# Optimization experiments

Hardware: AMD Instinct MI355X
Metric: run time of the kernel (lower is better)

The kernel has to match this reference:

```python
import jax, jax.numpy as jnp
import numpy as np

B, N, IN_DIM = 64, 4096, 128
D = 128          # slot_size
S = 7            # num_slots
ITERS = 3
HID = 256        # mlp_hdim
EPS = 1e-8       # renorm epsilon
LN_EPS = 1e-5    # torch LayerNorm default


def _ln(x, g, b):
    m = jnp.mean(x, axis=-1, keepdims=True)
    v = jnp.mean((x - m) ** 2, axis=-1, keepdims=True)
    return (x - m) * jax.lax.rsqrt(v + LN_EPS) * g + b


def setup_inputs() -> dict:
    key = jax.random.key(0)
    ks = jax.random.split(key, 16)
    s = 0.02
    return {
        "x": jax.random.normal(ks[0], (B, N, IN_DIM), jnp.float32),
        "noise": jax.random.normal(ks[1], (B, S, D), jnp.float32),
        "Wq": jax.random.normal(ks[2], (D, D), jnp.float32) * s,
        "Wk": jax.random.normal(ks[3], (D, IN_DIM), jnp.float32) * s,
        "Wv": jax.random.normal(ks[4], (D, IN_DIM), jnp.float32) * s,
        "ln_in_g": jnp.ones((IN_DIM,), jnp.float32),
        "ln_in_b": jnp.zeros((IN_DIM,), jnp.float32),
        "ln_slots_g": jnp.ones((D,), jnp.float32),
        "ln_slots_b": jnp.zeros((D,), jnp.float32),
        "ln_mlp_g": jnp.ones((D,), jnp.float32),
        "ln_mlp_b": jnp.zeros((D,), jnp.float32),
        "W_ih": jax.random.normal(ks[5], (3 * D, D), jnp.float32) * s,
        "W_hh": jax.random.normal(ks[6], (3 * D, D), jnp.float32) * s,
        "b_ih": jnp.zeros((3 * D,), jnp.float32),
        "b_hh": jnp.zeros((3 * D,), jnp.float32),
        "W1": jax.random.normal(ks[7], (HID, D), jnp.float32) * s,
        "b1": jnp.zeros((HID,), jnp.float32),
        "W2": jax.random.normal(ks[8], (D, HID), jnp.float32) * s,
        "b2": jnp.zeros((D,), jnp.float32),
        "mu": jax.random.normal(ks[9], (1, 1, D), jnp.float32) * s,
        "logsigma": jax.random.normal(ks[10], (1, D), jnp.float32) * s,
    }


def reference(x, noise, Wq, Wk, Wv, ln_in_g, ln_in_b, ln_slots_g, ln_slots_b,
              ln_mlp_g, ln_mlp_b, W_ih, W_hh, b_ih, b_hh, W1, b1, W2, b2,
              mu, logsigma):
    xn = _ln(x, ln_in_g, ln_in_b)              # (B,N,IN)
    k = xn @ Wk.T                              # (B,N,D)
    v = xn @ Wv.T                              # (B,N,D)

    scale = jax.nn.softplus(logsigma)[None] + 1e-5   # (1,1,D)
    slots = mu + scale * noise                 # rsample, (B,S,D)

    def gru(u, h):
        gx = u @ W_ih.T + b_ih                 # (B*S, 3D)
        gh = h @ W_hh.T + b_hh
        xr, xz, xn_ = jnp.split(gx, 3, axis=-1)
        hr, hz, hn = jnp.split(gh, 3, axis=-1)
        r = jax.nn.sigmoid(xr + hr)
        z = jax.nn.sigmoid(xz + hz)
        n = jnp.tanh(xn_ + r * hn)
        return (1.0 - z) * n + z * h

    inv_sqrt_d = D ** -0.5
    for _ in range(ITERS):
        slots_prev = slots
        sn = _ln(slots, ln_slots_g, ln_slots_b)
        q = sn @ Wq.T                          # (B,S,D)
        scores = inv_sqrt_d * jnp.einsum('bnd,bsd->bns', k, q)
        attn = jax.nn.softmax(scores, axis=-1)           # over slots
        attn = attn + EPS
        attn = attn / jnp.sum(attn, axis=1, keepdims=True)  # renorm over inputs
        updates = jnp.einsum('bns,bnd->bsd', attn, v)    # (B,S,D)
        h = gru(updates.reshape(-1, D), slots_prev.reshape(-1, D))
        slots = h.reshape(x.shape[0], S, D)
        slots = _ln(slots, ln_mlp_g, ln_mlp_b)
        slots = slots + (jax.nn.relu(slots @ W1.T + b1) @ W2.T + b2)
    return slots
```

## Files before the change

### kernel.cpp

```cpp
#include <hip/hip_runtime.h>
#include <hip/hip_bf16.h>
#include <stdint.h>

#define B_ 64
#define N_ 4096
#define D_ 128
#define S_ 7
#define EPS_ 1e-8f
#define LN_EPS_ 1e-5f
#define SC_INV 0.08838834764831843f

typedef float  f32x4  __attribute__((ext_vector_type(4)));
typedef __bf16 bf16x8 __attribute__((ext_vector_type(8)));

#define WIH_OFF 0
#define WHH_OFF 49152
#define W1_OFF  98304
#define W2_OFF  131072
#define WQ_OFF  163840
#define WKT_OFF 180224
#define WV_OFF  196608
#define WBF_TOT 212992

__device__ __forceinline__ uint16_t f2bfbits(float f) {
    uint32_t x = __float_as_uint(f);
    return (uint16_t)((x + 0x7fffu + ((x >> 16) & 1u)) >> 16);
}
__device__ __forceinline__ uint32_t pk2(float a, float b) {
    return (uint32_t)f2bfbits(a) | ((uint32_t)f2bfbits(b) << 16);
}

__global__ __launch_bounds__(256) void k_init_prep(
    const float* __restrict__ noise, const float* __restrict__ Wk,
    const float* __restrict__ mu, const float* __restrict__ logsigma,
    const float* __restrict__ Wq, const float* __restrict__ lsg,
    const float* __restrict__ lsb,
    const float* __restrict__ Wih, const float* __restrict__ Whh,
    const float* __restrict__ W1, const float* __restrict__ W2,
    const float* __restrict__ Wv,
    float* __restrict__ slots, uint16_t* __restrict__ kqbf,
    uint16_t* __restrict__ wbf,
    const float* __restrict__ x, const float* __restrict__ lng,
    const float* __restrict__ lnb, uint16_t* __restrict__ xn) {
    const int t = threadIdx.x;
    if (blockIdx.x < 448) {
        __shared__ float sn[128], qr[128];
        __shared__ float red[2];
        const int tid = blockIdx.x * 256 + t;
        const int row = blockIdx.x;
        const int b = row / 7, s = row - b * 7;
        bool act = t < 128;
        float v = 0.f;
        if (act) {
            float sc = log1pf(__expf(logsigma[t])) + 1e-5f;
            v = mu[t] + sc * noise[row * 128 + t];
            slots[row * 128 + t] = v;
        }
        float sv = act ? v : 0.f;
        #pragma unroll
        for (int m = 1; m < 64; m <<= 1) sv += __shfl_xor(sv, m);
        if (act && (t & 63) == 0) red[t >> 6] = sv;
        __syncthreads();
        float mean = (red[0] + red[1]) * (1.0f / 128.0f);
        __syncthreads();
        float dv = act ? (v - mean) : 0.f;
        float sq = dv * dv;
        #pragma unroll
        for (int m = 1; m < 64; m <<= 1) sq += __shfl_xor(sq, m);
        if (act && (t & 63) == 0) red[t >> 6] = sq;
        __syncthreads();
        float var = (red[0] + red[1]) * (1.0f / 128.0f);
        if (act) sn[t] = dv * rsqrtf(var + LN_EPS_) * lsg[t] + lsb[t];
        __syncthreads();
        if (act) {
            const float4* wr = (const float4*)(Wq + t * 128);
            float acc = 0.f;
            #pragma unroll 8
            for (int j = 0; j < 32; ++j) {
                float4 w = wr[j];
                float4 s4 = *(const float4*)(sn + 4 * j);
                acc += w.x * s4.x + w.y * s4.y + w.z * s4.z + w.w * s4.w;
            }
            qr[t] = acc;
        }
        __syncthreads();
        if (act) {
            float kq = 0.f;
            #pragma unroll 8
            for (int o = 0; o < 128; ++o) kq += qr[o] * Wk[o * 128 + t];
            int elem = (t >> 5) * 512 + (s + 16 * ((t >> 3) & 3)) * 8 + (t & 7);
            kqbf[b * 2048 + elem] = f2bfbits(kq * SC_INV);
        }
        if (tid < 73728) {
            int bb = tid / 1152, rem = tid - bb * 1152;
            int sp = 7 + (rem >> 7), d = rem & 127;
            int elem = (d >> 5) * 512 + (sp + 16 * ((d >> 3) & 3)) * 8 + (d & 7);
            kqbf[bb * 2048 + elem] = 0;
        }
        for (int e = tid; e < WBF_TOT; e += 448 * 256) {
            const float* W; int C, el, mode = 0;
            if (e < WHH_OFF)      { W = Wih; C = 128; el = e; }
            else if (e < W1_OFF)  { W = Whh; C = 128; el = e - WHH_OFF; }
            else if (e < W2_OFF)  { W = W1;  C = 128; el = e - W1_OFF; }
            else if (e < WQ_OFF)  { W = W2;  C = 256; el = e - W2_OFF; }
            else if (e < WKT_OFF) { W = Wq;  C = 128; el = e - WQ_OFF; }
            else if (e < WV_OFF)  { W = Wk;  C = 128; el = e - WKT_OFF; mode = 1; }
            else                  { W = Wv;  C = 128; el = e - WV_OFF; }
            int tile = el >> 9, within = el & 511;
            int lp = within >> 3, j = within & 7;
            int lm_ = lp & 15, qd_ = lp >> 4;
            float w;
            if (!mode) {
                int ktN = C >> 5, ot = tile / ktN, kt = tile - ot * ktN;
                w = W[(ot * 16 + lm_) * C + kt * 32 + qd_ * 8 + j];
            } else {
                int dt = tile >> 2, kt = tile & 3;
                w = W[(kt * 32 + qd_ * 8 + j) * 128 + dt * 16 + lm_];
            }
            wbf[e] = f2bfbits(w);
        }
        return;
    }
    const int pid = blockIdx.x - 448;
    const int wv = t >> 6, lane = t & 63;
    const int lm = lane & 15, qd = lane >> 4;
    const long row = (long)pid * 64 + wv * 16 + lm;
    const long ntile = (long)pid * 4 + wv;
    const float* xp = x + row * 128 + qd * 4;
    f32x4 xa[8];
    #pragma unroll
    for (int c = 0; c < 8; ++c) xa[c] = *(const f32x4*)(xp + c * 16);
    float s = 0.f, sq = 0.f;
    #pragma unroll
    for (int c = 0; c < 8; ++c)
        #pragma unroll
        for (int r = 0; r < 4; ++r) { float v = xa[c][r]; s += v; sq += v * v; }
    s  += __shfl_xor(s, 16);  s  += __shfl_xor(s, 32);
    sq += __shfl_xor(sq, 16); sq += __shfl_xor(sq, 32);
    float mean = s * (1.0f / 128.0f);
    float var  = sq * (1.0f / 128.0f) - mean * mean;
    float rs   = rsqrtf(var + LN_EPS_);
    #pragma unroll
    for (int c = 0; c < 8; ++c) {
        f32x4 g  = *(const f32x4*)(lng + c * 16 + qd * 4);
        f32x4 bb = *(const f32x4*)(lnb + c * 16 + qd * 4);
        float v0 = (xa[c][0] - mean) * rs * g[0] + bb[0];
        float v1 = (xa[c][1] - mean) * rs * g[1] + bb[1];
        float v2 = (xa[c][2] - mean) * rs * g[2] + bb[2];
        float v3 = (xa[c][3] - mean) * rs * g[3] + bb[3];
        uint2 st; st.x = pk2(v0, v1); st.y = pk2(v2, v3);
        long elem = (ntile * 4 + (c >> 1)) * 512
                  + (lm + 16 * (2 * (c & 1) + (qd >> 1))) * 8 + 4 * (qd & 1);
        *(uint2*)(xn + elem) = st;
    }
}

__global__ __launch_bounds__(256, 4) void k_attn(
    const uint16_t* __restrict__ xn, const uint16_t* __restrict__ kqbf,
    float* __restrict__ upart, float* __restrict__ cpart) {
    __shared__ __align__(16) uint16_t stage[4][32 * 132];
    __shared__ __align__(16) uint16_t als[4][16 * 36];
    __shared__ float bsum[4][8];
    const int t = threadIdx.x, wv = t >> 6, lane = t & 63;
    const int lm = lane & 15, qd = lane >> 4;
    const int b = blockIdx.x >> 4, chunk = blockIdx.x & 15;
    const int ntb = b * 256 + chunk * 16 + wv * 4;
    const int sbase = qd * 4;

    bf16x8 kqf[4];
    #pragma unroll
    for (int k0 = 0; k0 < 4; ++k0)
        kqf[k0] = *(const bf16x8*)(kqbf + b * 2048 + k0 * 512 + lane * 8);

    uint16_t* xw = stage[wv];
    float* prt = (float*)stage[wv];
    uint16_t* aw = als[wv];
    f32x4 uacc[8];
    #pragma unroll
    for (int i = 0; i < 8; ++i) uacc[i] = (f32x4){0.f, 0.f, 0.f, 0.f};
    f32x4 csl = {0.f, 0.f, 0.f, 0.f};

    #pragma unroll
    for (int sub = 0; sub < 2; ++sub) {
        bf16x8 xf[2][4];
        #pragma unroll
        for (int nt = 0; nt < 2; ++nt)
            #pragma unroll
            for (int k0 = 0; k0 < 4; ++k0)
                xf[nt][k0] = *(const bf16x8*)(xn +
                    ((long)(ntb + sub * 2 + nt) * 4 + k0) * 512 + lane * 8);
        #pragma unroll
        for (int nt = 0; nt < 2; ++nt)
            #pragma unroll
            for (int k0 = 0; k0 < 4; ++k0) {
                int base = (nt * 16 + lm) * 132 + k0 * 32 + qd * 8;
                const uint2* src = (const uint2*)&xf[nt][k0];
                *(uint2*)(xw + base)     = src[0];
                *(uint2*)(xw + base + 4) = src[1];
            }
        f32x4 sc[2];
        #pragma unroll
        for (int nt = 0; nt < 2; ++nt) {
            f32x4 acc = {0.f, 0.f, 0.f, 0.f};
            #pragma unroll
            for (int k0 = 0; k0 < 4; ++k0)
                acc = __builtin_amdgcn_mfma_f32_16x16x32_bf16(kqf[k0], xf[nt][k0], acc, 0, 0, 0);
            sc[nt] = acc;
        }
        #pragma unroll
        for (int nt = 0; nt < 2; ++nt) {
            float mx = -1e30f;
            #pragma unroll
            for (int r = 0; r < 4; ++r)
                if (sbase + r < 7) mx = fmaxf(mx, sc[nt][r]);
            mx = fmaxf(mx, __shfl_xor(mx, 16));
            mx = fmaxf(mx, __shfl_xor(mx, 32));
            float e[4], tot = 0.f;
            #pragma unroll
            for (int r = 0; r < 4; ++r) {
                e[r] = (sbase + r < 7) ? __expf(sc[nt][r] - mx) : 0.f;
                tot += e[r];
            }
            tot += __shfl_xor(tot, 16);
            tot += __shfl_xor(tot, 32);
            float inv = 1.0f / tot;
            #pragma unroll
            for (int r = 0; r < 4; ++r) {
                float a_ = (sbase + r < 7) ? e[r] * inv + EPS_ : 0.f;
                csl[r] += a_;
                aw[(sbase + r) * 36 + nt * 16 + lm] = f2bfbits(a_);
            }
        }
        union { uint2 u[2]; bf16x8 v; } cva;
        cva.u[0] = *(const uint2*)(aw + lm * 36 + qd * 8);
        cva.u[1] = *(const uint2*)(aw + lm * 36 + qd * 8 + 4);
        bf16x8 afr = cva.v;
        #pragma unroll
        for (int dt = 0; dt < 8; ++dt) {
            bf16x8 bfr;
            #pragma unroll
            for (int j = 0; j < 8; ++j)
                bfr[j] = ((const __bf16*)xw)[(qd * 8 + j) * 132 + dt * 16 + lm];
            uacc[dt] = __builtin_amdgcn_mfma_f32_16x16x32_bf16(afr, bfr, uacc[dt], 0, 0, 0);
        }
    }
    #pragma unroll
    for (int m = 1; m < 16; m <<= 1) {
        csl[0] += __shfl_xor(csl[0], m);
        csl[1] += __shfl_xor(csl[1], m);
        csl[2] += __shfl_xor(csl[2], m);
        csl[3] += __shfl_xor(csl[3], m);
    }
    if (lm == 0) {
        #pragma unroll
        for (int r = 0; r < 4; ++r) {
            int s = sbase + r;
            if (s < 7) bsum[wv][s] = csl[r];
        }
    }
    #pragma unroll
    for (int dt = 0; dt < 8; ++dt)
        #pragma unroll
        for (int r = 0; r < 4; ++r) {
            int s = sbase + r;
            if (s < 7) prt[s * 132 + dt * 16 + lm] = uacc[dt][r];
        }
    __syncthreads();
    if (t < 128) {
        const float* p0 = (const float*)stage[0];
        const float* p1 = (const float*)stage[1];
        const float* p2 = (const float*)stage[2];
        const float* p3 = (const float*)stage[3];
        #pragma unroll
        for (int s = 0; s < 7; ++s) {
            int o = s * 132 + t;
            upart[((b * 16 + chunk) * 7 + s) * 128 + t] = p0[o] + p1[o] + p2[o] + p3[o];
        }
    }
    if (t < 7)
        cpart[(b * 16 + chunk) * 7 + t] = bsum[0][t] + bsum[1][t] + bsum[2][t] + bsum[3][t];
}

__global__ __launch_bounds__(256) void k_fused(
    const float* __restrict__ upart, const float* __restrict__ cpart,
    float* __restrict__ slots, const uint16_t* __restrict__ wbf,
    const float* __restrict__ bih, const float* __restrict__ bhh,
    const float* __restrict__ gm, const float* __restrict__ bm,
    const float* __restrict__ b1, const float* __restrict__ b2,
    const float* __restrict__ lsg, const float* __restrict__ lsb,
    uint16_t* __restrict__ kqbf, float* __restrict__ dst, int hasq) {
    __shared__ float uf[16][132];
    __shared__ float hf[16][132];
    __shared__ float slf[16][132];
    __shared__ float hidl[16][264];
    __shared__ float glg[7][776];
    __shared__ float csl[7];
    const int b = blockIdx.x;
    const int t = threadIdx.x, wv = t >> 6, lane = t & 63;
    const int lm = lane & 15, qd = lane >> 4;

    if (t < 7) {
        float c = 0.f;
        #pragma unroll
        for (int i = 0; i < 16; ++i) c += cpart[(b * 16 + i) * 7 + t];
        csl[t] = c;
    }
    for (int idx = t; idx < 896; idx += 256) {
        int s = idx >> 7, d = idx & 127;
        float acc = 0.f;
        #pragma unroll
        for (int i = 0; i < 16; ++i) acc += upart[((b * 16 + i) * 7 + s) * 128 + d];
        slf[s][d] = acc;
        hf[s][d] = slots[(b * 7 + s) * 128 + d];
    }
    __syncthreads();

    {
        bf16x8 apb[4];
        #pragma unroll
        for (int k0 = 0; k0 < 4; ++k0)
            #pragma unroll
            for (int j = 0; j < 8; ++j) apb[k0][j] = (__bf16)slf[lm][k0 * 32 + qd * 8 + j];
        #pragma unroll
        for (int i = 0; i < 2; ++i) {
            int dt = wv * 2 + i;
            f32x4 acc = {0.f, 0.f, 0.f, 0.f};
            #pragma unroll
            for (int k0 = 0; k0 < 4; ++k0) {
                bf16x8 bf = *(const bf16x8*)(wbf + WV_OFF + ((dt * 4 + k0) << 9) + lane * 8);
                acc = __builtin_amdgcn_mfma_f32_16x16x32_bf16(apb[k0], bf, acc, 0, 0, 0);
            }
            #pragma unroll
            for (int r = 0; r < 4; ++r) {
                int s = qd * 4 + r;
                if (s < 7) uf[s][dt * 16 + lm] = acc[r] / csl[s];
            }
        }
    }
    __syncthreads();

    bf16x8 au[4], ah[4];
    #pragma unroll
    for (int k0 = 0; k0 < 4; ++k0)
        #pragma unroll
        for (int j = 0; j < 8; ++j) {
            au[k0][j] = (__bf16)uf[lm][k0 * 32 + qd * 8 + j];
            ah[k0][j] = (__bf16)hf[lm][k0 * 32 + qd * 8 + j];
        }
    {
        const int ih = (wv < 2);
        const uint16_t* W = wbf + (ih ? WIH_OFF : WHH_OFF);
        const int base = ih ? 0 : 384;
        const int w2 = wv & 1;
        #pragma unroll
        for (int i = 0; i < 12; ++i) {
            int ot = w2 * 12 + i;
            f32x4 acc = {0.f, 0.f, 0.f, 0.f};
            #pragma unroll
            for (int k0 = 0; k0 < 4; ++k0) {
                bf16x8 bf = *(const bf16x8*)(W + ((ot * 4 + k0) << 9) + lane * 8);
                acc = __builtin_amdgcn_mfma_f32_16x16x32_bf16(ih ? au[k0] : ah[k0], bf, acc, 0, 0, 0);
            }
            #pragma unroll
            for (int r = 0; r < 4; ++r) {
                int s = qd * 4 + r;
                if (s < 7) glg[s][base + ot * 16 + lm] = acc[r];
            }
        }
    }
    __syncthreads();

    for (int idx = t; idx < 896; idx += 256) {
        int s = idx >> 7, d = idx & 127;
        float xr = glg[s][d] + bih[d];
        float xz = glg[s][128 + d] + bih[128 + d];
        float xg = glg[s][256 + d] + bih[256 + d];
        float hr = glg[s][384 + d] + bhh[d];
        float hz = glg[s][512 + d] + bhh[128 + d];
        float hg = glg[s][640 + d] + bhh[256 + d];
        float r = 1.f / (1.f + __expf(-(xr + hr)));
        float z = 1.f / (1.f + __expf(-(xz + hz)));
        float n = tanhf(xg + r * hg);
        uf[s][d] = (1.f - z) * n + z * hf[s][d];
    }
    __syncthreads();

    for (int s = wv; s < 7; s += 4) {
        float a0 = uf[s][2 * lane], a1 = uf[s][2 * lane + 1];
        float sm = a0 + a1, sq = a0 * a0 + a1 * a1;
        #pragma unroll
        for (int m = 1; m < 64; m <<= 1) { sm += __shfl_xor(sm, m); sq += __shfl_xor(sq, m); }
        float mean = sm * (1.0f / 128.0f);
        float var = sq * (1.0f / 128.0f) - mean * mean;
        float rs = rsqrtf(var + LN_EPS_);
        slf[s][2 * lane]     = (a0 - mean) * rs * gm[2 * lane] + bm[2 * lane];
        slf[s][2 * lane + 1] = (a1 - mean) * rs * gm[2 * lane + 1] + bm[2 * lane + 1];
    }
    __syncthreads();

    bf16x8 as_[4];
    #pragma unroll
    for (int k0 = 0; k0 < 4; ++k0)
        #pragma unroll
        for (int j = 0; j < 8; ++j) as_[k0][j] = (__bf16)slf[lm][k0 * 32 + qd * 8 + j];
    #pragma unroll
    for (int i = 0; i < 4; ++i) {
        int ot = wv * 4 + i;
        f32x4 acc = {0.f, 0.f, 0.f, 0.f};
        #pragma unroll
        for (int k0 = 0; k0 < 4; ++k0) {
            bf16x8 bf = *(const bf16x8*)(wbf + W1_OFF + ((ot * 4 + k0) << 9) + lane * 8);
            acc = __builtin_amdgcn_mfma_f32_16x16x32_bf16(as_[k0], bf, acc, 0, 0, 0);
        }
        #pragma unroll
        for (int r = 0; r < 4; ++r) {
            int s = qd * 4 + r;
            if (s < 7) hidl[s][ot * 16 + lm] = fmaxf(acc[r] + b1[ot * 16 + lm], 0.f);
        }
    }
    __syncthreads();

    bf16x8 ahd[8];
    #pragma unroll
    for (int k0 = 0; k0 < 8; ++k0)
        #pragma unroll
        for (int j = 0; j < 8; ++j) ahd[k0][j] = (__bf16)hidl[lm][k0 * 32 + qd * 8 + j];
    #pragma unroll
    for (int i = 0; i < 2; ++i) {
        int ot = wv * 2 + i;
        f32x4 acc = {0.f, 0.f, 0.f, 0.f};
        #pragma unroll
        for (int k0 = 0; k0 < 8; ++k0) {
            bf16x8 bf = *(const bf16x8*)(wbf + W2_OFF + ((ot * 8 + k0) << 9) + lane * 8);
            acc = __builtin_amdgcn_mfma_f32_16x16x32_bf16(ahd[k0], bf, acc, 0, 0, 0);
        }
        #pragma unroll
        for (int r = 0; r < 4; ++r) {
            int s = qd * 4 + r;
            if (s < 7) {
                float v = slf[s][ot * 16 + lm] + acc[r] + b2[ot * 16 + lm];
                hf[s][ot * 16 + lm] = v;
                dst[(b * 7 + s) * 128 + ot * 16 + lm] = v;
            }
        }
    }
    if (hasq) {
        __syncthreads();
        for (int s = wv; s < 7; s += 4) {
            float a0 = hf[s][2 * lane], a1 = hf[s][2 * lane + 1];
            float sm = a0 + a1, sq = a0 * a0 + a1 * a1;
            #pragma unroll
            for (int m = 1; m < 64; m <<= 1) { sm += __shfl_xor(sm, m); sq += __shfl_xor(sq, m); }
            float mean = sm * (1.0f / 128.0f);
            float var = sq * (1.0f / 128.0f) - mean * mean;
            float rs = rsqrtf(var + LN_EPS_);
            uf[s][2 * lane]     = (a0 - mean) * rs * lsg[2 * lane] + lsb[2 * lane];
            uf[s][2 * lane + 1] = (a1 - mean) * rs * lsg[2 * lane + 1] + lsb[2 * lane + 1];
        }
        __syncthreads();
        bf16x8 an[4];
        #pragma unroll
        for (int k0 = 0; k0 < 4; ++k0)
            #pragma unroll
            for (int j = 0; j < 8; ++j) an[k0][j] = (__bf16)uf[lm][k0 * 32 + qd * 8 + j];
        #pragma unroll
        for (int i = 0; i < 2; ++i) {
            int ot = wv * 2 + i;
            f32x4 acc = {0.f, 0.f, 0.f, 0.f};
            #pragma unroll
            for (int k0 = 0; k0 < 4; ++k0) {
                bf16x8 bf = *(const bf16x8*)(wbf + WQ_OFF + ((ot * 4 + k0) << 9) + lane * 8);
                acc = __builtin_amdgcn_mfma_f32_16x16x32_bf16(an[k0], bf, acc, 0, 0, 0);
            }
            #pragma unroll
            for (int r = 0; r < 4; ++r) {
                int s = qd * 4 + r;
                if (s < 7) slf[s][ot * 16 + lm] = acc[r];
            }
        }
        __syncthreads();
        bf16x8 aq[4];
        #pragma unroll
        for (int k0 = 0; k0 < 4; ++k0)
            #pragma unroll
            for (int j = 0; j < 8; ++j) aq[k0][j] = (__bf16)slf[lm][k0 * 32 + qd * 8 + j];
        #pragma unroll
        for (int i = 0; i < 2; ++i) {
            int dt = wv * 2 + i;
            f32x4 acc = {0.f, 0.f, 0.f, 0.f};
            #pragma unroll
            for (int k0 = 0; k0 < 4; ++k0) {
                bf16x8 bf = *(const bf16x8*)(wbf + WKT_OFF + ((dt * 4 + k0) << 9) + lane * 8);
                acc = __builtin_amdgcn_mfma_f32_16x16x32_bf16(aq[k0], bf, acc, 0, 0, 0);
            }
            #pragma unroll
            for (int r = 0; r < 4; ++r) {
                int s = qd * 4 + r;
                if (s < 7) hidl[s][dt * 16 + lm] = acc[r];
            }
        }
        __syncthreads();
        {
            int kt = t >> 6, lp = t & 63;
            int lmp = lp & 15, qdp = lp >> 4;
            uint16_t h[8];
            #pragma unroll
            for (int j = 0; j < 8; ++j)
                h[j] = (lmp < 7) ? f2bfbits(hidl[lmp][kt * 32 + qdp * 8 + j] * SC_INV) : (uint16_t)0;
            uint4 st;
            st.x = (uint32_t)h[0] | ((uint32_t)h[1] << 16);
            st.y = (uint32_t)h[2] | ((uint32_t)h[3] << 16);
            st.z = (uint32_t)h[4] | ((uint32_t)h[5] << 16);
            st.w = (uint32_t)h[6] | ((uint32_t)h[7] << 16);
            *(uint4*)(kqbf + b * 2048 + t * 8) = st;
        }
    }
}

extern "C" void kernel_launch(void* const* d_in, const int* in_sizes, int n_in,
                              void* d_out, int out_size, void* d_ws, size_t ws_size,
                              hipStream_t stream) {
    const float* x    = (const float*)d_in[0];
    const float* nz   = (const float*)d_in[1];
    const float* Wq   = (const float*)d_in[2];
    const float* Wk   = (const float*)d_in[3];
    const float* Wv   = (const float*)d_in[4];
    const float* ling = (const float*)d_in[5];
    const float* linb = (const float*)d_in[6];
    const float* lsg  = (const float*)d_in[7];
    const float* lsb  = (const float*)d_in[8];
    const float* lmg  = (const float*)d_in[9];
    const float* lmb  = (const float*)d_in[10];
    const float* Wih  = (const float*)d_in[11];
    const float* Whh  = (const float*)d_in[12];
    const float* bih  = (const float*)d_in[13];
    const float* bhh  = (const float*)d_in[14];
    const float* W1   = (const float*)d_in[15];
    const float* b1   = (const float*)d_in[16];
    const float* W2   = (const float*)d_in[17];
    const float* b2   = (const float*)d_in[18];
    const float* mu   = (const float*)d_in[19];
    const float* lsig = (const float*)d_in[20];

    char* wsb = (char*)d_ws;
    uint16_t* xn    = (uint16_t*)(wsb);
    uint16_t* wbf   = (uint16_t*)(wsb + (size_t)67108864);
    uint16_t* kqbf  = (uint16_t*)(wsb + (size_t)67534848);
    float*    slots = (float*)  (wsb + (size_t)67796992);
    float*    upart = (float*)  (wsb + (size_t)68026368);
    float*    cpart = (float*)  (wsb + (size_t)71696384);

    k_init_prep<<<4544, 256, 0, stream>>>(nz, Wk, mu, lsig, Wq, lsg, lsb,
                                          Wih, Whh, W1, W2, Wv, slots, kqbf, wbf,
                                          x, ling, linb, xn);
    for (int it = 0; it < 3; ++it) {
        float* dst = (it == 2) ? (float*)d_out : slots;
        k_attn<<<1024, 256, 0, stream>>>(xn, kqbf, upart, cpart);
        k_fused<<<64, 256, 0, stream>>>(upart, cpart, slots, wbf, bih, bhh,
                                        lmg, lmb, b1, b2, lsg, lsb,
                                        kqbf, dst, (it < 2) ? 1 : 0);
    }
}
```

Baseline: 352.8 us.

## Fuse slot-update tail into attention kernel via last-block atomic counter

Merges the per-iteration attention kernel and the per-batch GRU/MLP/query kernel into one launch. Each batch's 16 chunk blocks increment an atomic counter, and the last one to finish reduces the partials and runs the slot update and next-query computation. This removes three kernel launches and the gap between each pair of kernels. In exchange it adds threadfences and atomics, aliases shared memory between the two phases, and the tail work now runs in whichever block finishes last, which may serialize behind other blocks.

```diff
diff --git a/kernel.cpp b/kernel.cpp
--- a/kernel.cpp
+++ b/kernel.cpp
@@ -39,7 +39,7 @@
     const float* __restrict__ W1, const float* __restrict__ W2,
     const float* __restrict__ Wv,
     float* __restrict__ slots, uint16_t* __restrict__ kqbf,
-    uint16_t* __restrict__ wbf,
+    uint16_t* __restrict__ wbf, int* __restrict__ ctr,
     const float* __restrict__ x, const float* __restrict__ lng,
     const float* __restrict__ lnb, uint16_t* __restrict__ xn) {
     const int t = threadIdx.x;
@@ -49,6 +49,7 @@
         const int tid = blockIdx.x * 256 + t;
         const int row = blockIdx.x;
         const int b = row / 7, s = row - b * 7;
+        if (tid < 192) ctr[tid] = 0;
         bool act = t < 128;
         float v = 0.f;
         if (act) {
@@ -155,364 +156,380 @@
     }
 }
 
-__global__ __launch_bounds__(256, 4) void k_attn(
-    const uint16_t* __restrict__ xn, const uint16_t* __restrict__ kqbf,
-    float* __restrict__ upart, float* __restrict__ cpart) {
-    __shared__ __align__(16) uint16_t stage[4][32 * 132];
-    __shared__ __align__(16) uint16_t als[4][16 * 36];
-    __shared__ float bsum[4][8];
-    const int t = threadIdx.x, wv = t >> 6, lane = t & 63;
-    const int lm = lane & 15, qd = lane >> 4;
-    const int b = blockIdx.x >> 4, chunk = blockIdx.x & 15;
-    const int ntb = b * 256 + chunk * 16 + wv * 4;
-    const int sbase = qd * 4;
-
-    bf16x8 kqf[4];
-    #pragma unroll
-    for (int k0 = 0; k0 < 4; ++k0)
-        kqf[k0] = *(const bf16x8*)(kqbf + b * 2048 + k0 * 512 + lane * 8);
-
-    uint16_t* xw = stage[wv];
-    float* prt = (float*)stage[wv];
-    uint16_t* aw = als[wv];
-    f32x4 uacc[8];
-    #pragma unroll
-    for (int i = 0; i < 8; ++i) uacc[i] = (f32x4){0.f, 0.f, 0.f, 0.f};
-    f32x4 csl = {0.f, 0.f, 0.f, 0.f};
-
-    #pragma unroll
-    for (int sub = 0; sub < 2; ++sub) {
-        bf16x8 xf[2][4];
-        #pragma unroll
-        for (int nt = 0; nt < 2; ++nt)
-            #pragma unroll
-            for (int k0 = 0; k0 < 4; ++k0)
-                xf[nt][k0] = *(const bf16x8*)(xn +
-                    ((long)(ntb + sub * 2 + nt) * 4 + k0) * 512 + lane * 8);
-        #pragma unroll
-        for (int nt = 0; nt < 2; ++nt)
-            #pragma unroll
-            for (int k0 = 0; k0 < 4; ++k0) {
-                int base = (nt * 16 + lm) * 132 + k0 * 32 + qd * 8;
-                const uint2* src = (const uint2*)&xf[nt][k0];
-                *(uint2*)(xw + base)     = src[0];
-                *(uint2*)(xw + base + 4) = src[1];
-            }
-        f32x4 sc[2];
-        #pragma unroll
-        for (int nt = 0; nt < 2; ++nt) {
-            f32x4 acc = {0.f, 0.f, 0.f, 0.f};
-            #pragma unroll
-            for (int k0 = 0; k0 < 4; ++k0)
-                acc = __builtin_amdgcn_mfma_f32_16x16x32_bf16(kqf[k0], xf[nt][k0], acc, 0, 0, 0);
-            sc[nt] = acc;
-        }
-        #pragma unroll
-        for (int nt = 0; nt < 2; ++nt) {
-            float mx = -1e30f;
-            #pragma unroll
-            for (int r = 0; r < 4; ++r)
-                if (sbase + r < 7) mx = fmaxf(mx, sc[nt][r]);
-            mx = fmaxf(mx, __shfl_xor(mx, 16));
-            mx = fmaxf(mx, __shfl_xor(mx, 32));
-            float e[4], tot = 0.f;
-            #pragma unroll
-            for (int r = 0; r < 4; ++r) {
-                e[r] = (sbase + r < 7) ? __expf(sc[nt][r] - mx) : 0.f;
-                tot += e[r];
-            }
-            tot += __shfl_xor(tot, 16);
-            tot += __shfl_xor(tot, 32);
-            float inv = 1.0f / tot;
-            #pragma unroll
-            for (int r = 0; r < 4; ++r) {
-                float a_ = (sbase + r < 7) ? e[r] * inv + EPS_ : 0.f;
-                csl[r] += a_;
-                aw[(sbase + r) * 36 + nt * 16 + lm] = f2bfbits(a_);
-            }
-        }
-        union { uint2 u[2]; bf16x8 v; } cva;
-        cva.u[0] = *(const uint2*)(aw + lm * 36 + qd * 8);
-        cva.u[1] = *(const uint2*)(aw + lm * 36 + qd * 8 + 4);
-        bf16x8 afr = cva.v;
-        #pragma unroll
-        for (int dt = 0; dt < 8; ++dt) {
-            bf16x8 bfr;
-            #pragma unroll
-            for (int j = 0; j < 8; ++j)
-                bfr[j] = ((const __bf16*)xw)[(qd * 8 + j) * 132 + dt * 16 + lm];
-            uacc[dt] = __builtin_amdgcn_mfma_f32_16x16x32_bf16(afr, bfr, uacc[dt], 0, 0, 0);
-        }
-    }
-    #pragma unroll
-    for (int m = 1; m < 16; m <<= 1) {
-        csl[0] += __shfl_xor(csl[0], m);
-        csl[1] += __shfl_xor(csl[1], m);
-        csl[2] += __shfl_xor(csl[2], m);
-        csl[3] += __shfl_xor(csl[3], m);
-    }
-    if (lm == 0) {
-        #pragma unroll
-        for (int r = 0; r < 4; ++r) {
-            int s = sbase + r;
-            if (s < 7) bsum[wv][s] = csl[r];
-        }
-    }
-    #pragma unroll
-    for (int dt = 0; dt < 8; ++dt)
-        #pragma unroll
-        for (int r = 0; r < 4; ++r) {
-            int s = sbase + r;
-            if (s < 7) prt[s * 132 + dt * 16 + lm] = uacc[dt][r];
-        }
-    __syncthreads();
-    if (t < 128) {
-        const float* p0 = (const float*)stage[0];
-        const float* p1 = (const float*)stage[1];
-        const float* p2 = (const float*)stage[2];
-        const float* p3 = (const float*)stage[3];
-        #pragma unroll
-        for (int s = 0; s < 7; ++s) {
-            int o = s * 132 + t;
-            upart[((b * 16 + chunk) * 7 + s) * 128 + t] = p0[o] + p1[o] + p2[o] + p3[o];
-        }
-    }
-    if (t < 7)
-        cpart[(b * 16 + chunk) * 7 + t] = bsum[0][t] + bsum[1][t] + bsum[2][t] + bsum[3][t];
-}
-
-__global__ __launch_bounds__(256) void k_fused(
-    const float* __restrict__ upart, const float* __restrict__ cpart,
-    float* __restrict__ slots, const uint16_t* __restrict__ wbf,
+__global__ __launch_bounds__(256, 4) void k_attn_fused(
+    const uint16_t* __restrict__ xn, uint16_t* __restrict__ kqbf,
+    const uint16_t* __restrict__ wbf,
+    float* __restrict__ upart, float* __restrict__ cpart,
+    float* __restrict__ slots,
     const float* __restrict__ bih, const float* __restrict__ bhh,
     const float* __restrict__ gm, const float* __restrict__ bm,
     const float* __restrict__ b1, const float* __restrict__ b2,
     const float* __restrict__ lsg, const float* __restrict__ lsb,
-    uint16_t* __restrict__ kqbf, float* __restrict__ dst, int hasq) {
-    __shared__ float uf[16][132];
-    __shared__ float hf[16][132];
-    __shared__ float slf[16][132];
-    __shared__ float hidl[16][264];
-    __shared__ float glg[7][776];
-    __shared__ float csl[7];
-    const int b = blockIdx.x;
+    int* __restrict__ ctr, float* __restrict__ dstp, int hasq) {
+    __shared__ __align__(16) char smem[38528];
+    __shared__ int lastf;
+    uint16_t* stageA = (uint16_t*)smem;
+    uint16_t* alsA   = (uint16_t*)(smem + 33792);
+    float*    bsumA  = (float*)(smem + 38400);
+    float* slf  = (float*)smem;
+    float* uf   = (float*)(smem + 4224);
+    float* hf   = (float*)(smem + 8448);
+    float* glg  = (float*)(smem + 12672);
+    float* hidl = (float*)(smem + 12672);
+    float* cslf = (float*)(smem + 34176);
+
     const int t = threadIdx.x, wv = t >> 6, lane = t & 63;
     const int lm = lane & 15, qd = lane >> 4;
-
-    if (t < 7) {
-        float c = 0.f;
-        #pragma unroll
-        for (int i = 0; i < 16; ++i) c += cpart[(b * 16 + i) * 7 + t];
-        csl[t] = c;
+    const int ab = blockIdx.x >> 4, chunk = blockIdx.x & 15;
+    const int ntb = ab * 256 + chunk * 16 + wv * 4;
+    const int sbase = qd * 4;
+
+    {
+        uint16_t* xw = stageA + wv * 4224;
+        float* prt = (float*)xw;
+        uint16_t* aw = alsA + wv * 576;
+        bf16x8 kqf[4];
+        #pragma unroll
+        for (int k0 = 0; k0 < 4; ++k0)
+            kqf[k0] = *(const bf16x8*)(kqbf + ab * 2048 + k0 * 512 + lane * 8);
+        f32x4 uacc[8];
+        #pragma unroll
+        for (int i = 0; i < 8; ++i) uacc[i] = (f32x4){0.f, 0.f, 0.f, 0.f};
+        f32x4 csl = {0.f, 0.f, 0.f, 0.f};
+
+        #pragma unroll
+        for (int sub = 0; sub < 2; ++sub) {
+            bf16x8 xf[2][4];
+            #pragma unroll
+            for (int nt = 0; nt < 2; ++nt)
+                #pragma unroll
+                for (int k0 = 0; k0 < 4; ++k0)
+                    xf[nt][k0] = *(const bf16x8*)(xn +
+                        ((long)(ntb + sub * 2 + nt) * 4 + k0) * 512 + lane * 8);
+            #pragma unroll
+            for (int nt = 0; nt < 2; ++nt)
+                #pragma unroll
+                for (int k0 = 0; k0 < 4; ++k0) {
+                    int base = (nt * 16 + lm) * 132 + k0 * 32 + qd * 8;
+                    const uint2* src = (const uint2*)&xf[nt][k0];
+                    *(uint2*)(xw + base)     = src[0];
+                    *(uint2*)(xw + base + 4) = src[1];
+                }
+            f32x4 sc[2];
+            #pragma unroll
+            for (int nt = 0; nt < 2; ++nt) {
+                f32x4 acc = {0.f, 0.f, 0.f, 0.f};
+                #pragma unroll
+                for (int k0 = 0; k0 < 4; ++k0)
+                    acc = __builtin_amdgcn_mfma_f32_16x16x32_bf16(kqf[k0], xf[nt][k0], acc, 0, 0, 0);
+                sc[nt] = acc;
+            }
+            #pragma unroll
+            for (int nt = 0; nt < 2; ++nt) {
+                float mx = -1e30f;
+                #pragma unroll
+                for (int r = 0; r < 4; ++r)
+                    if (sbase + r < 7) mx = fmaxf(mx, sc[nt][r]);
+                mx = fmaxf(mx, __shfl_xor(mx, 16));
+                mx = fmaxf(mx, __shfl_xor(mx, 32));
+                float e[4], tot = 0.f;
+                #pragma unroll
+                for (int r = 0; r < 4; ++r) {
+                    e[r] = (sbase + r < 7) ? __expf(sc[nt][r] - mx) : 0.f;
+                    tot += e[r];
+                }
+                tot += __shfl_xor(tot, 16);
+                tot += __shfl_xor(tot, 32);
+                float inv = 1.0f / tot;
+                #pragma unroll
+                for (int r = 0; r < 4; ++r) {
+                    float a_ = (sbase + r < 7) ? e[r] * inv + EPS_ : 0.f;
+                    csl[r] += a_;
+                    aw[(sbase + r) * 36 + nt * 16 + lm] = f2bfbits(a_);
+                }
+            }
+            union { uint2 u[2]; bf16x8 v; } cva;
+            cva.u[0] = *(const uint2*)(aw + lm * 36 + qd * 8);
+            cva.u[1] = *(const uint2*)(aw + lm * 36 + qd * 8 + 4);
+            bf16x8 afr = cva.v;
+            #pragma unroll
+            for (int dt = 0; dt < 8; ++dt) {
+                bf16x8 bfr;
+                #pragma unroll
+                for (int j = 0; j < 8; ++j)
+                    bfr[j] = ((const __bf16*)xw)[(qd * 8 + j) * 132 + dt * 16 + lm];
+                uacc[dt] = __builtin_amdgcn_mfma_f32_16x16x32_bf16(afr, bfr, uacc[dt], 0, 0, 0);
+            }
+        }
+        #pragma unroll
+        for (int m = 1; m < 16; m <<= 1) {
+            csl[0] += __shfl_xor(csl[0], m);
+            csl[1] += __shfl_xor(csl[1], m);
+            csl[2] += __shfl_xor(csl[2], m);
+            csl[3] += __shfl_xor(csl[3], m);
+        }
+        if (lm == 0) {
+            #pragma unroll
+            for (int r = 0; r < 4; ++r) {
+                int s = sbase + r;
+                if (s < 7) bsumA[wv * 8 + s] = csl[r];
+            }
+        }
+        #pragma unroll
+        for (int dt = 0; dt < 8; ++dt)
+            #pragma unroll
+            for (int r = 0; r < 4; ++r) {
+                int s = sbase + r;
+                if (s < 7) prt[s * 132 + dt * 16 + lm] = uacc[dt][r];
+            }
+        __syncthreads();
+        if (t < 128) {
+            const float* p0 = (const float*)(stageA);
+            const float* p1 = (const float*)(stageA + 4224);
+            const float* p2 = (const float*)(stageA + 8448);
+            const float* p3 = (const float*)(stageA + 12672);
+            #pragma unroll
+            for (int s = 0; s < 7; ++s) {
+                int o = s * 132 + t;
+                upart[((ab * 16 + chunk) * 7 + s) * 128 + t] = p0[o] + p1[o] + p2[o] + p3[o];
+            }
+        }
+        if (t < 7)
+            cpart[(ab * 16 + chunk) * 7 + t] =
+                bsumA[0 * 8 + t] + bsumA[1 * 8 + t] + bsumA[2 * 8 + t] + bsumA[3 * 8 + t];
     }
-    for (int idx = t; idx < 896; idx += 256) {
-        int s = idx >> 7, d = idx & 127;
-        float acc = 0.f;
-        #pragma unroll
-        for (int i = 0; i < 16; ++i) acc += upart[((b * 16 + i) * 7 + s) * 128 + d];
-        slf[s][d] = acc;
-        hf[s][d] = slots[(b * 7 + s) * 128 + d];
+    __threadfence();
+    __syncthreads();
+    if (t == 0) {
+        int prev = atomicAdd(&ctr[ab], 1);
+        lastf = (prev == 15) ? 1 : 0;
     }
     __syncthreads();
-
+    if (!lastf) return;
+    __threadfence();
     {
-        bf16x8 apb[4];
+        const int fb = ab;
+        if (t < 7) {
+            float c = 0.f;
+            #pragma unroll
+            for (int i = 0; i < 16; ++i) c += cpart[(fb * 16 + i) * 7 + t];
+            cslf[t] = c;
+        }
+        for (int idx = t; idx < 896; idx += 256) {
+            int s = idx >> 7, d = idx & 127;
+            float acc = 0.f;
+            #pragma unroll
+            for (int i = 0; i < 16; ++i) acc += upart[((fb * 16 + i) * 7 + s) * 128 + d];
+            slf[s * 132 + d] = acc;
+            hf[s * 132 + d] = slots[(fb * 7 + s) * 128 + d];
+        }
+        __syncthreads();
+
+        {
+            bf16x8 apb[4];
+            #pragma unroll
+            for (int k0 = 0; k0 < 4; ++k0)
+                #pragma unroll
+                for (int j = 0; j < 8; ++j)
+                    apb[k0][j] = (__bf16)slf[(lm & 7) * 132 + k0 * 32 + qd * 8 + j];
+            #pragma unroll
+            for (int i = 0; i < 2; ++i) {
+                int dt = wv * 2 + i;
+                f32x4 acc = {0.f, 0.f, 0.f, 0.f};
+                #pragma unroll
+                for (int k0 = 0; k0 < 4; ++k0) {
+                    bf16x8 bf = *(const bf16x8*)(wbf + WV_OFF + ((dt * 4 + k0) << 9) + lane * 8);
+                    acc = __builtin_amdgcn_mfma_f32_16x16x32_bf16(apb[k0], bf, acc, 0, 0, 0);
+                }
+                #pragma unroll
+                for (int r = 0; r < 4; ++r) {
+                    int s = qd * 4 + r;
+                    if (s < 7) uf[s * 132 + dt * 16 + lm] = acc[r] / cslf[s];
+                }
+            }
+        }
+        __syncthreads();
+
+        bf16x8 au[4], ah[4];
         #pragma unroll
         for (int k0 = 0; k0 < 4; ++k0)
             #pragma unroll
-            for (int j = 0; j < 8; ++j) apb[k0][j] = (__bf16)slf[lm][k0 * 32 + qd * 8 + j];
-        #pragma unroll
-        for (int i = 0; i < 2; ++i) {
-            int dt = wv * 2 + i;
-            f32x4 acc = {0.f, 0.f, 0.f, 0.f};
-            #pragma unroll
-            for (int k0 = 0; k0 < 4; ++k0) {
-                bf16x8 bf = *(const bf16x8*)(wbf + WV_OFF + ((dt * 4 + k0) << 9) + lane * 8);
-                acc = __builtin_amdgcn_mfma_f32_16x16x32_bf16(apb[k0], bf, acc, 0, 0, 0);
-            }
-            #pragma unroll
-            for (int r = 0; r < 4; ++r) {
-                int s = qd * 4 + r;
-                if (s < 7) uf[s][dt * 16 + lm] = acc[r] / csl[s];
-            }
-        }
-    }
-    __syncthreads();
-
-    bf16x8 au[4], ah[4];
-    #pragma unroll
-    for (int k0 = 0; k0 < 4; ++k0)
-        #pragma unroll
-        for (int j = 0; j < 8; ++j) {
-            au[k0][j] = (__bf16)uf[lm][k0 * 32 + qd * 8 + j];
-            ah[k0][j] = (__bf16)hf[lm][k0 * 32 + qd * 8 + j];
-        }
-    {
-        const int ih = (wv < 2);
-        const uint16_t* W = wbf + (ih ? WIH_OFF : WHH_OFF);
-        const int base = ih ? 0 : 384;
-        const int w2 = wv & 1;
-        #pragma unroll
-        for (int i = 0; i < 12; ++i) {
-            int ot = w2 * 12 + i;
-            f32x4 acc = {0.f, 0.f, 0.f, 0.f};
-            #pragma unroll
-            for (int k0 = 0; k0 < 4; ++k0) {
-                bf16x8 bf = *(const bf16x8*)(W + ((ot * 4 + k0) << 9) + lane * 8);
-                acc = __builtin_amdgcn_mfma_f32_16x16x32_bf16(ih ? au[k0] : ah[k0], bf, acc, 0, 0, 0);
-            }
-            #pragma unroll
-            for (int r = 0; r < 4; ++r) {
-                int s = qd * 4 + r;
-                if (s < 7) glg[s][base + ot * 16 + lm] = acc[r];
-            }
-        }
-    }
-    __syncthreads();
-
-    for (int idx = t; idx < 896; idx += 256) {
-        int s = idx >> 7, d = idx & 127;
-        float xr = glg[s][d] + bih[d];
-        float xz = glg[s][128 + d] + bih[128 + d];
-        float xg = glg[s][256 + d] + bih[256 + d];
-        float hr = glg[s][384 + d] + bhh[d];
-        float hz = glg[s][512 + d] + bhh[128 + d];
-        float hg = glg[s][640 + d] + bhh[256 + d];
-        float r = 1.f / (1.f + __expf(-(xr + hr)));
-        float z = 1.f / (1.f + __expf(-(xz + hz)));
-        float n = tanhf(xg + r * hg);
-        uf[s][d] = (1.f - z) * n + z * hf[s][d];
-    }
-    __syncthreads();
-
-    for (int s = wv; s < 7; s += 4) {
-        float a0 = uf[s][2 * lane], a1 = uf[s][2 * lane + 1];
-        float sm = a0 + a1, sq = a0 * a0 + a1 * a1;
-        #pragma unroll
-        for (int m = 1; m < 64; m <<= 1) { sm += __shfl_xor(sm, m); sq += __shfl_xor(sq, m); }
-        float mean = sm * (1.0f / 128.0f);
-        float var = sq * (1.0f / 128.0f) - mean * mean;
-        float rs = rsqrtf(var + LN_EPS_);
-        slf[s][2 * lane]     = (a0 - mean) * rs * gm[2 * lane] + bm[2 * lane];
-        slf[s][2 * lane + 1] = (a1 - mean) * rs * gm[2 * lane + 1] + bm[2 * lane + 1];
-    }
-    __syncthreads();
-
-    bf16x8 as_[4];
-    #pragma unroll
-    for (int k0 = 0; k0 < 4; ++k0)
-        #pragma unroll
-        for (int j = 0; j < 8; ++j) as_[k0][j] = (__bf16)slf[lm][k0 * 32 + qd * 8 + j];
-    #pragma unroll
-    for (int i = 0; i < 4; ++i) {
-        int ot = wv * 4 + i;
-        f32x4 acc = {0.f, 0.f, 0.f, 0.f};
-        #pragma unroll
-        for (int k0 = 0; k0 < 4; ++k0) {
-            bf16x8 bf = *(const bf16x8*)(wbf + W1_OFF + ((ot * 4 + k0) << 9) + lane * 8);
-            acc = __builtin_amdgcn_mfma_f32_16x16x32_bf16(as_[k0], bf, acc, 0, 0, 0);
-        }
-        #pragma unroll
-        for (int r = 0; r < 4; ++r) {
-            int s = qd * 4 + r;
-            if (s < 7) hidl[s][ot * 16 + lm] = fmaxf(acc[r] + b1[ot * 16 + lm], 0.f);
-        }
-    }
-    __syncthreads();
-
-    bf16x8 ahd[8];
-    #pragma unroll
-    for (int k0 = 0; k0 < 8; ++k0)
-        #pragma unroll
-        for (int j = 0; j < 8; ++j) ahd[k0][j] = (__bf16)hidl[lm][k0 * 32 + qd * 8 + j];
-    #pragma unroll
-    for (int i = 0; i < 2; ++i) {
-        int ot = wv * 2 + i;
-        f32x4 acc = {0.f, 0.f, 0.f, 0.f};
-        #pragma unroll
-        for (int k0 = 0; k0 < 8; ++k0) {
-            bf16x8 bf = *(const bf16x8*)(wbf + W2_OFF + ((ot * 8 + k0) << 9) + lane * 8);
-            acc = __builtin_amdgcn_mfma_f32_16x16x32_bf16(ahd[k0], bf, acc, 0, 0, 0);
-        }
-        #pragma unroll
-        for (int r = 0; r < 4; ++r) {
-            int s = qd * 4 + r;
-            if (s < 7) {
-                float v = slf[s][ot * 16 + lm] + acc[r] + b2[ot * 16 + lm];
-                hf[s][ot * 16 + lm] = v;
-                dst[(b * 7 + s) * 128 + ot * 16 + lm] = v;
-            }
-        }
-    }
-    if (hasq) {
-        __syncthreads();
+            for (int j = 0; j < 8; ++j) {
+                au[k0][j] = (__bf16)uf[(lm & 7) * 132 + k0 * 32 + qd * 8 + j];
+                ah[k0][j] = (__bf16)hf[(lm & 7) * 132 + k0 * 32 + qd * 8 + j];
+            }
+        {
+            const int ih = (wv < 2);
+            const uint16_t* W = wbf + (ih ? WIH_OFF : WHH_OFF);
+            const int base = ih ? 0 : 384;
+            const int w2 = wv & 1;
+            #pragma unroll
+            for (int i = 0; i < 12; ++i) {
+                int ot = w2 * 12 + i;
+                f32x4 acc = {0.f, 0.f, 0.f, 0.f};
+                #pragma unroll
+                for (int k0 = 0; k0 < 4; ++k0) {
+                    bf16x8 bf = *(const bf16x8*)(W + ((ot * 4 + k0) << 9) + lane * 8);
+                    acc = __builtin_amdgcn_mfma_f32_16x16x32_bf16(ih ? au[k0] : ah[k0], bf, acc, 0, 0, 0);
+                }
+                #pragma unroll
+                for (int r = 0; r < 4; ++r) {
+                    int s = qd * 4 + r;
+                    if (s < 7) glg[s * 768 + base + ot * 16 + lm] = acc[r];
+                }
+            }
+        }
+        __syncthreads();
+
+        for (int idx = t; idx < 896; idx += 256) {
+            int s = idx >> 7, d = idx & 127;
+            float xr = glg[s * 768 + d] + bih[d];
+            float xz = glg[s * 768 + 128 + d] + bih[128 + d];
+            float xg = glg[s * 768 + 256 + d] + bih[256 + d];
+            float hr = glg[s * 768 + 384 + d] + bhh[d];
+            float hz = glg[s * 768 + 512 + d] + bhh[128 + d];
+            float hg = glg[s * 768 + 640 + d] + bhh[256 + d];
+            float r = 1.f / (1.f + __expf(-(xr + hr)));
+            float z = 1.f / (1.f + __expf(-(xz + hz)));
+            float n = tanhf(xg + r * hg);
+            uf[s * 132 + d] = (1.f - z) * n + z * hf[s * 132 + d];
+        }
+        __syncthreads();
+
         for (int s = wv; s < 7; s += 4) {
-            float a0 = hf[s][2 * lane], a1 = hf[s][2 * lane + 1];
+            float a0 = uf[s * 132 + 2 * lane], a1 = uf[s * 132 + 2 * lane + 1];
             float sm = a0 + a1, sq = a0 * a0 + a1 * a1;
             #pragma unroll
             for (int m = 1; m < 64; m <<= 1) { sm += __shfl_xor(sm, m); sq += __shfl_xor(sq, m); }
             float mean = sm * (1.0f / 128.0f);
             float var = sq * (1.0f / 128.0f) - mean * mean;
             float rs = rsqrtf(var + LN_EPS_);
-            uf[s][2 * lane]     = (a0 - mean) * rs * lsg[2 * lane] + lsb[2 * lane];
-            uf[s][2 * lane + 1] = (a1 - mean) * rs * lsg[2 * lane + 1] + lsb[2 * lane + 1];
-        }
-        __syncthreads();
-        bf16x8 an[4];
+            slf[s * 132 + 2 * lane]     = (a0 - mean) * rs * gm[2 * lane] + bm[2 * lane];
+            slf[s * 132 + 2 * lane + 1] = (a1 - mean) * rs * gm[2 * lane + 1] + bm[2 * lane + 1];
+        }
+        __syncthreads();
+
+        bf16x8 as_[4];
         #pragma unroll
         for (int k0 = 0; k0 < 4; ++k0)
             #pragma unroll
-            for (int j = 0; j < 8; ++j) an[k0][j] = (__bf16)uf[lm][k0 * 32 + qd * 8 + j];
+            for (int j = 0; j < 8; ++j)
+                as_[k0][j] = (__bf16)slf[(lm & 7) * 132 + k0 * 32 + qd * 8 + j];
+        #pragma unroll
+        for (int i = 0; i < 4; ++i) {
+            int ot = wv * 4 + i;
+            f32x4 acc = {0.f, 0.f, 0.f, 0.f};
+            #pragma unroll
+            for (int k0 = 0; k0 < 4; ++k0) {
+                bf16x8 bf = *(const bf16x8*)(wbf + W1_OFF + ((ot * 4 + k0) << 9) + lane * 8);
+                acc = __builtin_amdgcn_mfma_f32_16x16x32_bf16(as_[k0], bf, acc, 0, 0, 0);
+            }
+            #pragma unroll
+            for (int r = 0; r < 4; ++r) {
+                int s = qd * 4 + r;
+                if (s < 7) hidl[s * 264 + ot * 16 + lm] = fmaxf(acc[r] + b1[ot * 16 + lm], 0.f);
+            }
+        }
+        __syncthreads();
+
+        bf16x8 ahd[8];
+        #pragma unroll
+        for (int k0 = 0; k0 < 8; ++k0)
+            #pragma unroll
+            for (int j = 0; j < 8; ++j)
+                ahd[k0][j] = (__bf16)hidl[(lm & 7) * 264 + k0 * 32 + qd * 8 + j];
         #pragma unroll
         for (int i = 0; i < 2; ++i) {
             int ot = wv * 2 + i;
             f32x4 acc = {0.f, 0.f, 0.f, 0.f};
             #pragma unroll
-            for (int k0 = 0; k0 < 4; ++k0) {
-                bf16x8 bf = *(const bf16x8*)(wbf + WQ_OFF + ((ot * 4 + k0) << 9) + lane * 8);
-                acc = __builtin_amdgcn_mfma_f32_16x16x32_bf16(an[k0], bf, acc, 0, 0, 0);
+            for (int k0 = 0; k0 < 8; ++k0) {
+                bf16x8 bf = *(const bf16x8*)(wbf + W2_OFF + ((ot * 8 + k0) << 9) + lane * 8);
+                acc = __builtin_amdgcn_mfma_f32_16x16x32_bf16(ahd[k0], bf, acc, 0, 0, 0);
             }
             #pragma unroll
             for (int r = 0; r < 4; ++r) {
                 int s = qd * 4 + r;
-                if (s < 7) slf[s][ot * 16 + lm] = acc[r];
-            }
-        }
-        __syncthreads();
-        bf16x8 aq[4];
-        #pragma unroll
-        for (int k0 = 0; k0 < 4; ++k0)
-            #pragma unroll
-            for (int j = 0; j < 8; ++j) aq[k0][j] = (__bf16)slf[lm][k0 * 32 + qd * 8 + j];
-        #pragma unroll
-        for (int i = 0; i < 2; ++i) {
-            int dt = wv * 2 + i;
-            f32x4 acc = {0.f, 0.f, 0.f, 0.f};
-            #pragma unroll
-            for (int k0 = 0; k0 < 4; ++k0) {
-                bf16x8 bf = *(const bf16x8*)(wbf + WKT_OFF + ((dt * 4 + k0) << 9) + lane * 8);
-                acc = __builtin_amdgcn_mfma_f32_16x16x32_bf16(aq[k0], bf, acc, 0, 0, 0);
-            }
-            #pragma unroll
-            for (int r = 0; r < 4; ++r) {
-                int s = qd * 4 + r;
-                if (s < 7) hidl[s][dt * 16 + lm] = acc[r];
-            }
-        }
-        __syncthreads();
-        {
-            int kt = t >> 6, lp = t & 63;
-            int lmp = lp & 15, qdp = lp >> 4;
-            uint16_t h[8];
-            #pragma unroll
-            for (int j = 0; j < 8; ++j)
-                h[j] = (lmp < 7) ? f2bfbits(hidl[lmp][kt * 32 + qdp * 8 + j] * SC_INV) : (uint16_t)0;
-            uint4 st;
-            st.x = (uint32_t)h[0] | ((uint32_t)h[1] << 16);
-            st.y = (uint32_t)h[2] | ((uint32_t)h[3] << 16);
-            st.z = (uint32_t)h[4] | ((uint32_t)h[5] << 16);
-            st.w = (uint32_t)h[6] | ((uint32_t)h[7] << 16);
-            *(uint4*)(kqbf + b * 2048 + t * 8) = st;
+                if (s < 7) {
+                    float v = slf[s * 132 + ot * 16 + lm] + acc[r] + b2[ot * 16 + lm];
+                    hf[s * 132 + ot * 16 + lm] = v;
+                    dstp[(fb * 7 + s) * 128 + ot * 16 + lm] = v;
+                }
+            }
+        }
+        if (hasq) {
+            __syncthreads();
+            for (int s = wv; s < 7; s += 4) {
+                float a0 = hf[s * 132 + 2 * lane], a1 = hf[s * 132 + 2 * lane + 1];
+                float sm = a0 + a1, sq = a0 * a0 + a1 * a1;
+                #pragma unroll
+                for (int m = 1; m < 64; m <<= 1) { sm += __shfl_xor(sm, m); sq += __shfl_xor(sq, m); }
+                float mean = sm * (1.0f / 128.0f);
+                float var = sq * (1.0f / 128.0f) - mean * mean;
+                float rs = rsqrtf(var + LN_EPS_);
+                uf[s * 132 + 2 * lane]     = (a0 - mean) * rs * lsg[2 * lane] + lsb[2 * lane];
+                uf[s * 132 + 2 * lane + 1] = (a1 - mean) * rs * lsg[2 * lane + 1] + lsb[2 * lane + 1];
+            }
+            __syncthreads();
+            bf16x8 an[4];
+            #pragma unroll
+            for (int k0 = 0; k0 < 4; ++k0)
+                #pragma unroll
+                for (int j = 0; j < 8; ++j)
+                    an[k0][j] = (__bf16)uf[(lm & 7) * 132 + k0 * 32 + qd * 8 + j];
+            #pragma unroll
+            for (int i = 0; i < 2; ++i) {
+                int ot = wv * 2 + i;
+                f32x4 acc = {0.f, 0.f, 0.f, 0.f};
+                #pragma unroll
+                for (int k0 = 0; k0 < 4; ++k0) {
+                    bf16x8 bf = *(const bf16x8*)(wbf + WQ_OFF + ((ot * 4 + k0) << 9) + lane * 8);
+                    acc = __builtin_amdgcn_mfma_f32_16x16x32_bf16(an[k0], bf, acc, 0, 0, 0);
+                }
+                #pragma unroll
+                for (int r = 0; r < 4; ++r) {
+                    int s = qd * 4 + r;
+                    if (s < 7) slf[s * 132 + ot * 16 + lm] = acc[r];
+                }
+            }
+            __syncthreads();
+            bf16x8 aq[4];
+            #pragma unroll
+            for (int k0 = 0; k0 < 4; ++k0)
+                #pragma unroll
+                for (int j = 0; j < 8; ++j)
+                    aq[k0][j] = (__bf16)slf[(lm & 7) * 132 + k0 * 32 + qd * 8 + j];
+            #pragma unroll
+            for (int i = 0; i < 2; ++i) {
+                int dt = wv * 2 + i;
+                f32x4 acc = {0.f, 0.f, 0.f, 0.f};
+                #pragma unroll
+                for (int k0 = 0; k0 < 4; ++k0) {
+                    bf16x8 bf = *(const bf16x8*)(wbf + WKT_OFF + ((dt * 4 + k0) << 9) + lane * 8);
+                    acc = __builtin_amdgcn_mfma_f32_16x16x32_bf16(aq[k0], bf, acc, 0, 0, 0);
+                }
+                #pragma unroll
+                for (int r = 0; r < 4; ++r) {
+                    int s = qd * 4 + r;
+                    if (s < 7) hidl[s * 264 + dt * 16 + lm] = acc[r];
+                }
+            }
+            __syncthreads();
+            {
+                int kt = t >> 6, lp = t & 63;
+                int lmp = lp & 15, qdp = lp >> 4;
+                uint16_t h[8];
+                #pragma unroll
+                for (int j = 0; j < 8; ++j)
+                    h[j] = (lmp < 7) ? f2bfbits(hidl[lmp * 264 + kt * 32 + qdp * 8 + j] * SC_INV)
+                                     : (uint16_t)0;
+                uint4 st;
+                st.x = (uint32_t)h[0] | ((uint32_t)h[1] << 16);
+                st.y = (uint32_t)h[2] | ((uint32_t)h[3] << 16);
+                st.z = (uint32_t)h[4] | ((uint32_t)h[5] << 16);
+                st.w = (uint32_t)h[6] | ((uint32_t)h[7] << 16);
+                *(uint4*)(kqbf + fb * 2048 + t * 8) = st;
+            }
         }
     }
 }
@@ -549,15 +566,15 @@
     float*    slots = (float*)  (wsb + (size_t)67796992);
     float*    upart = (float*)  (wsb + (size_t)68026368);
     float*    cpart = (float*)  (wsb + (size_t)71696384);
+    int*      ctr   = (int*)    (wsb + (size_t)71725056);
 
     k_init_prep<<<4544, 256, 0, stream>>>(nz, Wk, mu, lsig, Wq, lsg, lsb,
                                           Wih, Whh, W1, W2, Wv, slots, kqbf, wbf,
-                                          x, ling, linb, xn);
+                                          ctr, x, ling, linb, xn);
     for (int it = 0; it < 3; ++it) {
-        float* dst = (it == 2) ? (float*)d_out : slots;
-        k_attn<<<1024, 256, 0, stream>>>(xn, kqbf, upart, cpart);
-        k_fused<<<64, 256, 0, stream>>>(upart, cpart, slots, wbf, bih, bhh,
-                                        lmg, lmb, b1, b2, lsg, lsb,
-                                        kqbf, dst, (it < 2) ? 1 : 0);
+        float* dstp = (it == 2) ? (float*)d_out : slots;
+        k_attn_fused<<<1024, 256, 0, stream>>>(xn, kqbf, wbf, upart, cpart, slots,
+                                               bih, bhh, lmg, lmb, b1, b2, lsg, lsb,
+                                               ctr + it * 64, dstp, (it < 2) ? 1 : 0);
     }
 }
```

Measured after the change: 677.9 us. 92.2% more time.
